# Kernel tuning notes

Measured on AMD Instinct MI355X. Metric: run time of the kernel, lower is better.

Reference implementation:

```python
import jax, jax.numpy as jnp
import numpy as np

CAPS_N, DIMS_N, ROUNDS = 10, 16, 3
IN_CAPS_N, IN_DIMS_N = 1152, 8
BATCH = 256
EPS = 1e-7  # keras backend.epsilon()


def squash(x, axis=-1):
    sq = jnp.sum(x * x, axis=axis, keepdims=True)
    return (sq / (1.0 + sq)) * x / jnp.sqrt(sq + EPS)


def setup_inputs() -> dict:
    key = jax.random.key(0)
    k1, k2 = jax.random.split(key)
    inputs = jax.random.normal(k1, (BATCH, IN_CAPS_N, IN_DIMS_N), dtype=jnp.float32)
    # glorot-ish scale for the transform weights
    W = jax.random.normal(k2, (CAPS_N, IN_CAPS_N, DIMS_N, IN_DIMS_N), dtype=jnp.float32) * 0.05
    return {"inputs": inputs, "W": W}


def reference(inputs, W):
    # u_hat[b,j,i,d] = W[j,i] @ inputs[b,i]  (per-pair prediction vectors)
    u_hat = jnp.einsum('jide,bie->bjid', W, inputs)  # [B, caps_n, in_caps_n, dims_n]
    B = inputs.shape[0]
    cc = jnp.zeros((B, CAPS_N, IN_CAPS_N), dtype=u_hat.dtype)  # routing logits
    v = None
    for r in range(ROUNDS):
        c = jax.nn.softmax(cc, axis=1)                    # softmax over output capsules
        s = jnp.einsum('bji,bjid->bjd', c, u_hat)         # weighted sum over input caps
        v = squash(s, axis=-1)                            # [B, caps_n, dims_n]
        if r != ROUNDS - 1:
            cc = cc + jnp.einsum('bjid,bjd->bji', u_hat, v)  # agreement
    return v
```

## Files before the change

kernel.cpp:

```cpp
#include <hip/hip_runtime.h>

#define B_N 256
#define IC_N 1152
#define J_N 10
#define D_N 16

typedef __attribute__((ext_vector_type(8))) short short8;
typedef __attribute__((ext_vector_type(4))) float floatx4;

union u4s8 { uint4 u; short8 s; };

__device__ __forceinline__ float bf_lo(unsigned int u){
  union { unsigned int i; float f; } c; c.i = u << 16; return c.f;
}
__device__ __forceinline__ float bf_hi(unsigned int u){
  union { unsigned int i; float f; } c; c.i = u & 0xffff0000u; return c.f;
}
__device__ __forceinline__ unsigned int rne16(float f){
  union { float ff; unsigned int i; } c; c.ff = f;
  return (c.i + 0x7FFFu + ((c.i >> 16) & 1u)) >> 16;
}
__device__ __forceinline__ unsigned int pack_rne(float lo, float hi){
  return rne16(lo) | (rne16(hi) << 16);
}
__device__ __forceinline__ unsigned int pack_trunc(float lo, float hi){
  union { float f; unsigned int u; } a, b; a.f = lo; b.f = hi;
  return __builtin_amdgcn_perm(b.u, a.u, 0x07060302u);
}

__global__ __launch_bounds__(256) void caps_prep(
    const float* __restrict__ W, const float* __restrict__ x,
    uint4* __restrict__ wsf, uint4* __restrict__ wcc2,
    uint4* __restrict__ xbf, float* __restrict__ vsum)
{
  __shared__ unsigned int tx[4][64 * 17];
  const int blk = blockIdx.x, tid = threadIdx.x;
  if (blk < 720) {
    const int t = blk * 256 + tid;
    if (t < B_N * J_N * D_N) vsum[t] = 0.f;
    const int d  = t & 15;
    const int ji = t >> 4;
    const int i  = ji % IC_N;
    const int j  = ji / IC_N;
    const float4* src = (const float4*)(W + ((size_t)t << 3));
    const float4 a = src[0], b = src[1];
    uint4 q;
    q.x = pack_rne(a.x, a.y); q.y = pack_rne(a.z, a.w);
    q.z = pack_rne(b.x, b.y); q.w = pack_rne(b.z, b.w);
    wsf[(j * 288 + (i >> 2)) * 64 + (i & 3) * 16 + d] = q;
  } else if (blk < 1440) {
    const int t2    = (blk - 720) * 256 + tid;
    const int lane  = t2 & 31;
    const int rest  = t2 >> 5;
    const int itile = rest % 72;
    const int je    = rest / 72;
    const int e     = je & 7;
    const int j     = je >> 3;
    const int i     = itile * 16 + (lane & 15);
    const int dbase = (lane >> 4) * 8;
    const float* src = W + (((size_t)(j * IC_N + i) * D_N + dbase) << 3) + e;
    uint4 q;
    q.x = pack_rne(src[0],  src[8]);  q.y = pack_rne(src[16], src[24]);
    q.z = pack_rne(src[32], src[40]); q.w = pack_rne(src[48], src[56]);
    wcc2[t2] = q;
  } else {
    const int xb = blk - 1440;
    const int b0 = (xb / 18) * 16;
    const int i0 = (xb % 18) * 64;
    #pragma unroll
    for (int r = 0; r < 4; ++r) {
      const int bl = r * 4 + (tid >> 6);
      const int il = tid & 63;
      const float4* sp = (const float4*)(x + ((size_t)((b0 + bl) * IC_N + i0 + il) << 3));
      const float4 a = sp[0], c = sp[1];
      tx[0][il * 17 + bl] = pack_rne(a.x, a.y);
      tx[1][il * 17 + bl] = pack_rne(a.z, a.w);
      tx[2][il * 17 + bl] = pack_rne(c.x, c.y);
      tx[3][il * 17 + bl] = pack_rne(c.z, c.w);
    }
    __syncthreads();
    #pragma unroll
    for (int it = 0; it < 4; ++it) {
      const int p  = it * 256 + tid;
      const int il = p >> 4, bl = p & 15;
      uint4 q;
      q.x = tx[0][il * 17 + bl]; q.y = tx[1][il * 17 + bl];
      q.z = tx[2][il * 17 + bl]; q.w = tx[3][il * 17 + bl];
      xbf[(size_t)(i0 + il) * 256 + b0 + bl] = q;
    }
  }
}

__global__ __launch_bounds__(640, 5) void caps_pass(
    const uint4* __restrict__ xbf,
    const uint4* __restrict__ wsf,
    const uint4* __restrict__ wcc2,
    const uint4* __restrict__ vsbf,
    float* __restrict__ s_part,
    const int round)
{
  __shared__ float ccl[10 * 32 * 17];

  const int tid  = threadIdx.x;
  const int wave = tid >> 6;
  const int lane = tid & 63;
  const int quad = lane >> 4;
  const int col  = lane & 15;
  const int b0   = blockIdx.x << 4;
  const int i0   = blockIdx.y << 5;

  if (round > 0) {
    short8 av = {0,0,0,0,0,0,0,0};
    if (quad < 2)
      av = *(const short8*)&vsbf[((size_t)(b0 + col) * J_N + wave) * 2 + quad];

    #pragma unroll
    for (int t2 = 0; t2 < 2; ++t2) {
      uint4 bvq[8];
      #pragma unroll
      for (int e = 0; e < 8; ++e) {
        uint4 q = {0u, 0u, 0u, 0u};
        if (lane < 32)
          q = wcc2[(((size_t)wave * 8 + e) * 72 + (blockIdx.y << 1) + t2) * 32 + lane];
        bvq[e] = q;
      }
      uint4 xr[4];
      #pragma unroll
      for (int r = 0; r < 4; ++r)
        xr[r] = xbf[(size_t)(i0 + t2 * 16 + col) * 256 + b0 + quad * 4 + r];

      floatx4 cc4 = {0.f, 0.f, 0.f, 0.f};
      #pragma unroll
      for (int e = 0; e < 8; ++e) {
        u4s8 bv; bv.u = bvq[e];
        floatx4 tf = {0.f, 0.f, 0.f, 0.f};
        tf = __builtin_amdgcn_mfma_f32_16x16x32_bf16(av, bv.s, tf, 0, 0, 0);
        #pragma unroll
        for (int r = 0; r < 4; ++r) {
          const unsigned int u = ((const unsigned int*)&xr[r])[e >> 1];
          const float xe = (e & 1) ? bf_hi(u) : bf_lo(u);
          cc4[r] += tf[r] * xe;
        }
      }
      #pragma unroll
      for (int r = 0; r < 4; ++r)
        ccl[(wave * 32 + t2 * 16 + col) * 17 + quad * 4 + r] = cc4[r];
    }
    __syncthreads();
    if (tid < 512) {
      const int i = tid >> 4, b = tid & 15;
      float cc[10];
      #pragma unroll
      for (int j = 0; j < 10; ++j) cc[j] = ccl[(j * 32 + i) * 17 + b];
      float m = cc[0];
      #pragma unroll
      for (int j = 1; j < 10; ++j) m = fmaxf(m, cc[j]);
      float den = 0.f;
      #pragma unroll
      for (int j = 0; j < 10; ++j) { cc[j] = __expf(cc[j] - m); den += cc[j]; }
      const float rd = __builtin_amdgcn_rcpf(den);
      #pragma unroll
      for (int j = 0; j < 10; ++j) ccl[(j * 32 + i) * 17 + b] = cc[j] * rd;
    }
    __syncthreads();
  }

  floatx4 acc = {0.f, 0.f, 0.f, 0.f};
  #pragma unroll
  for (int g = 0; g < 2; ++g) {
    uint4 xq[4], wf[4];
    float cv[4];
    #pragma unroll
    for (int k = 0; k < 4; ++k) {
      const int kt = g * 4 + k;
      const int il = kt * 4 + quad;
      xq[k] = xbf[(size_t)(i0 + il) * 256 + b0 + col];
      wf[k] = wsf[((size_t)wave * 288 + (blockIdx.y << 3) + kt) * 64 + lane];
      cv[k] = (round > 0) ? ccl[(wave * 32 + il) * 17 + col] : 0.1f;
    }
    #pragma unroll
    for (int k = 0; k < 4; ++k) {
      short8 af;
      unsigned int* aq = (unsigned int*)&af;
      aq[0] = pack_trunc(bf_lo(xq[k].x) * cv[k], bf_hi(xq[k].x) * cv[k]);
      aq[1] = pack_trunc(bf_lo(xq[k].y) * cv[k], bf_hi(xq[k].y) * cv[k]);
      aq[2] = pack_trunc(bf_lo(xq[k].z) * cv[k], bf_hi(xq[k].z) * cv[k]);
      aq[3] = pack_trunc(bf_lo(xq[k].w) * cv[k], bf_hi(xq[k].w) * cv[k]);
      u4s8 bw; bw.u = wf[k];
      acc = __builtin_amdgcn_mfma_f32_16x16x32_bf16(af, bw.s, acc, 0, 0, 0);
    }
  }
  float* sp = s_part + ((((size_t)blockIdx.x * 10 + wave) * 16 + quad * 4) * 36
                        + blockIdx.y) * 16 + col;
  #pragma unroll
  for (int r = 0; r < 4; ++r) sp[r * 576] = acc[r];
}

__global__ __launch_bounds__(256) void caps_squash(
    const float* __restrict__ s_part, float* __restrict__ vsum,
    unsigned int* __restrict__ vsbf_u, float* __restrict__ out, const int round)
{
  const int tid  = threadIdx.x;
  const int w    = tid >> 6;
  const int lane = tid & 63;
  const int bj   = blockIdx.x * 4 + w;
  const int b    = bj / 10, j = bj - b * 10;
  const int btile = b >> 4, brem = b & 15;
  const float* base = s_part + (((size_t)btile * 10 + j) * 16 + brem) * 576;
  float acc = 0.f;
  #pragma unroll
  for (int q = 0; q < 9; ++q) acc += base[q * 64 + lane];
  acc += __shfl_xor(acc, 16, 64);
  acc += __shfl_xor(acc, 32, 64);
  const float s = acc;
  float sq = s * s;
  sq += __shfl_xor(sq, 1, 16);
  sq += __shfl_xor(sq, 2, 16);
  sq += __shfl_xor(sq, 4, 16);
  sq += __shfl_xor(sq, 8, 16);
  const float coef = (sq / (1.f + sq)) * rsqrtf(sq + 1e-7f);
  const float v = coef * s;
  if (round < 2) {
    const float vprev = (lane < 16) ? vsum[bj * 16 + lane] : 0.f;
    const float vt = vprev + v;
    const float vtn = __shfl_down(vt, 1, 64);
    if (lane < 16) {
      vsum[bj * 16 + lane] = vt;
      if (!(lane & 1))
        vsbf_u[bj * 8 + (lane >> 1)] = pack_rne(vt, vtn);
    }
  } else if (lane < 16) {
    out[bj * 16 + lane] = v;
  }
}

extern "C" void kernel_launch(void* const* d_in, const int* in_sizes, int n_in,
                              void* d_out, int out_size, void* d_ws, size_t ws_size,
                              hipStream_t stream)
{
  const float* x = (const float*)d_in[0];
  const float* W = (const float*)d_in[1];

  uint4* wsf   = (uint4*)d_ws;
  uint4* wcc2  = wsf + 184320;
  uint4* xbf   = wcc2 + 184320;
  float* s_prt = (float*)(xbf + 294912);
  float* vsum  = s_prt + 1474560;
  unsigned int* vsbf_u = (unsigned int*)(vsum + 40960);

  caps_prep<<<dim3(1728), dim3(256), 0, stream>>>(W, x, wsf, wcc2,
                                                  (uint4*)xbf, vsum);
  for (int r = 0; r < 3; ++r) {
    caps_pass<<<dim3(16, 36), dim3(640), 0, stream>>>(
        xbf, wsf, wcc2, (const uint4*)vsbf_u, s_prt, r);
    caps_squash<<<dim3(640), dim3(256), 0, stream>>>(
        s_prt, vsum, vsbf_u, (float*)d_out, r);
  }
}
```

Measured before the change: 131.0 us.

## Halve input-capsule tile per block, add batch-major x copy, fuse W prep via LDS

caps_pass now handles 16 input capsules per block instead of 32, doubling the grid to 16x72 blocks for more parallelism, and writes twice as many partial sums that caps_squash reduces over 18 chunks instead of 9. A second batch-major bf16 copy of x is produced so the agreement step reads coalesced rows. The W preprocessing is restructured so one block loads a 16-capsule W tile once into LDS and emits both the wsf and wcc2 layouts, cutting strided global reads. The cost is extra workspace, a larger partial-sum buffer and more reduction traffic in squash.

```diff
diff --git a/kernel.cpp b/kernel.cpp
--- a/kernel.cpp
+++ b/kernel.cpp
@@ -31,40 +31,49 @@
 __global__ __launch_bounds__(256) void caps_prep(
     const float* __restrict__ W, const float* __restrict__ x,
     uint4* __restrict__ wsf, uint4* __restrict__ wcc2,
-    uint4* __restrict__ xbf, float* __restrict__ vsum)
-{
-  __shared__ unsigned int tx[4][64 * 17];
-  const int blk = blockIdx.x, tid = threadIdx.x;
-  if (blk < 720) {
-    const int t = blk * 256 + tid;
-    if (t < B_N * J_N * D_N) vsum[t] = 0.f;
-    const int d  = t & 15;
-    const int ji = t >> 4;
-    const int i  = ji % IC_N;
-    const int j  = ji / IC_N;
-    const float4* src = (const float4*)(W + ((size_t)t << 3));
-    const float4 a = src[0], b = src[1];
-    uint4 q;
-    q.x = pack_rne(a.x, a.y); q.y = pack_rne(a.z, a.w);
-    q.z = pack_rne(b.x, b.y); q.w = pack_rne(b.z, b.w);
-    wsf[(j * 288 + (i >> 2)) * 64 + (i & 3) * 16 + d] = q;
-  } else if (blk < 1440) {
-    const int t2    = (blk - 720) * 256 + tid;
-    const int lane  = t2 & 31;
-    const int rest  = t2 >> 5;
-    const int itile = rest % 72;
-    const int je    = rest / 72;
-    const int e     = je & 7;
-    const int j     = je >> 3;
-    const int i     = itile * 16 + (lane & 15);
-    const int dbase = (lane >> 4) * 8;
-    const float* src = W + (((size_t)(j * IC_N + i) * D_N + dbase) << 3) + e;
-    uint4 q;
-    q.x = pack_rne(src[0],  src[8]);  q.y = pack_rne(src[16], src[24]);
-    q.z = pack_rne(src[32], src[40]); q.w = pack_rne(src[48], src[56]);
-    wcc2[t2] = q;
+    uint4* __restrict__ xbf_ib, uint4* __restrict__ xbf_bi,
+    float* __restrict__ vsum)
+{
+  const int tid = threadIdx.x;
+  if (blockIdx.x < 720) {
+    __shared__ unsigned int lw[1024];
+    const int j = blockIdx.x / 72, itile = blockIdx.x % 72;
+    const float4* Wt = (const float4*)(W + ((size_t)(j * IC_N + itile * 16) << 7));
+    #pragma unroll
+    for (int h = 0; h < 2; ++h) {
+      const float4 f = Wt[h * 256 + tid];
+      lw[(h * 256 + tid) * 2]     = pack_rne(f.x, f.y);
+      lw[(h * 256 + tid) * 2 + 1] = pack_rne(f.z, f.w);
+    }
+    __syncthreads();
+    {
+      const int ktl = tid >> 6, lane = tid & 63;
+      const int base = (ktl * 4 + (lane >> 4)) * 64 + (lane & 15) * 4;
+      uint4 q;
+      q.x = lw[base]; q.y = lw[base + 1]; q.z = lw[base + 2]; q.w = lw[base + 3];
+      wsf[((size_t)j * 288 + itile * 4 + ktl) * 64 + lane] = q;
+    }
+    {
+      const int e = tid >> 5, lane2 = tid & 31;
+      const int il = lane2 & 15, dbase = (lane2 >> 4) * 8;
+      unsigned short h[8];
+      #pragma unroll
+      for (int k = 0; k < 8; ++k) {
+        const unsigned int u = lw[il * 64 + (dbase + k) * 4 + (e >> 1)];
+        h[k] = (e & 1) ? (unsigned short)(u >> 16) : (unsigned short)(u & 0xffffu);
+      }
+      uint4 q;
+      q.x = h[0] | ((unsigned int)h[1] << 16);
+      q.y = h[2] | ((unsigned int)h[3] << 16);
+      q.z = h[4] | ((unsigned int)h[5] << 16);
+      q.w = h[6] | ((unsigned int)h[7] << 16);
+      wcc2[(((size_t)j * 8 + e) * 72 + itile) * 32 + lane2] = q;
+    }
   } else {
-    const int xb = blk - 1440;
+    __shared__ unsigned int tx[4][64 * 17];
+    const int xb = blockIdx.x - 720;
+    const int t0 = xb * 256 + tid;
+    if (t0 < B_N * J_N * D_N) vsum[t0] = 0.f;
     const int b0 = (xb / 18) * 16;
     const int i0 = (xb % 18) * 64;
     #pragma unroll
@@ -73,10 +82,12 @@
       const int il = tid & 63;
       const float4* sp = (const float4*)(x + ((size_t)((b0 + bl) * IC_N + i0 + il) << 3));
       const float4 a = sp[0], c = sp[1];
-      tx[0][il * 17 + bl] = pack_rne(a.x, a.y);
-      tx[1][il * 17 + bl] = pack_rne(a.z, a.w);
-      tx[2][il * 17 + bl] = pack_rne(c.x, c.y);
-      tx[3][il * 17 + bl] = pack_rne(c.z, c.w);
+      uint4 q;
+      q.x = pack_rne(a.x, a.y); q.y = pack_rne(a.z, a.w);
+      q.z = pack_rne(c.x, c.y); q.w = pack_rne(c.z, c.w);
+      xbf_bi[(size_t)(b0 + bl) * IC_N + i0 + il] = q;
+      tx[0][il * 17 + bl] = q.x; tx[1][il * 17 + bl] = q.y;
+      tx[2][il * 17 + bl] = q.z; tx[3][il * 17 + bl] = q.w;
     }
     __syncthreads();
     #pragma unroll
@@ -86,20 +97,21 @@
       uint4 q;
       q.x = tx[0][il * 17 + bl]; q.y = tx[1][il * 17 + bl];
       q.z = tx[2][il * 17 + bl]; q.w = tx[3][il * 17 + bl];
-      xbf[(size_t)(i0 + il) * 256 + b0 + bl] = q;
+      xbf_ib[(size_t)(i0 + il) * 256 + b0 + bl] = q;
     }
   }
 }
 
 __global__ __launch_bounds__(640, 5) void caps_pass(
-    const uint4* __restrict__ xbf,
+    const uint4* __restrict__ xbf_ib,
+    const uint4* __restrict__ xbf_bi,
     const uint4* __restrict__ wsf,
     const uint4* __restrict__ wcc2,
     const uint4* __restrict__ vsbf,
     float* __restrict__ s_part,
     const int round)
 {
-  __shared__ float ccl[10 * 32 * 17];
+  __shared__ float ccl[10 * 16 * 17];
 
   const int tid  = threadIdx.x;
   const int wave = tid >> 6;
@@ -107,51 +119,48 @@
   const int quad = lane >> 4;
   const int col  = lane & 15;
   const int b0   = blockIdx.x << 4;
-  const int i0   = blockIdx.y << 5;
+  const int i0   = blockIdx.y << 4;
 
   if (round > 0) {
     short8 av = {0,0,0,0,0,0,0,0};
     if (quad < 2)
       av = *(const short8*)&vsbf[((size_t)(b0 + col) * J_N + wave) * 2 + quad];
 
-    #pragma unroll
-    for (int t2 = 0; t2 < 2; ++t2) {
-      uint4 bvq[8];
-      #pragma unroll
-      for (int e = 0; e < 8; ++e) {
-        uint4 q = {0u, 0u, 0u, 0u};
-        if (lane < 32)
-          q = wcc2[(((size_t)wave * 8 + e) * 72 + (blockIdx.y << 1) + t2) * 32 + lane];
-        bvq[e] = q;
+    uint4 bvq[8];
+    #pragma unroll
+    for (int e = 0; e < 8; ++e) {
+      uint4 q = {0u, 0u, 0u, 0u};
+      if (lane < 32)
+        q = wcc2[(((size_t)wave * 8 + e) * 72 + blockIdx.y) * 32 + lane];
+      bvq[e] = q;
+    }
+    uint4 xr[4];
+    #pragma unroll
+    for (int r = 0; r < 4; ++r)
+      xr[r] = xbf_bi[(size_t)(b0 + quad * 4 + r) * IC_N + i0 + col];
+
+    floatx4 cc4 = {0.f, 0.f, 0.f, 0.f};
+    #pragma unroll
+    for (int e = 0; e < 8; ++e) {
+      u4s8 bv; bv.u = bvq[e];
+      floatx4 tf = {0.f, 0.f, 0.f, 0.f};
+      tf = __builtin_amdgcn_mfma_f32_16x16x32_bf16(av, bv.s, tf, 0, 0, 0);
+      #pragma unroll
+      for (int r = 0; r < 4; ++r) {
+        const unsigned int u = ((const unsigned int*)&xr[r])[e >> 1];
+        const float xe = (e & 1) ? bf_hi(u) : bf_lo(u);
+        cc4[r] += tf[r] * xe;
       }
-      uint4 xr[4];
-      #pragma unroll
-      for (int r = 0; r < 4; ++r)
-        xr[r] = xbf[(size_t)(i0 + t2 * 16 + col) * 256 + b0 + quad * 4 + r];
-
-      floatx4 cc4 = {0.f, 0.f, 0.f, 0.f};
-      #pragma unroll
-      for (int e = 0; e < 8; ++e) {
-        u4s8 bv; bv.u = bvq[e];
-        floatx4 tf = {0.f, 0.f, 0.f, 0.f};
-        tf = __builtin_amdgcn_mfma_f32_16x16x32_bf16(av, bv.s, tf, 0, 0, 0);
-        #pragma unroll
-        for (int r = 0; r < 4; ++r) {
-          const unsigned int u = ((const unsigned int*)&xr[r])[e >> 1];
-          const float xe = (e & 1) ? bf_hi(u) : bf_lo(u);
-          cc4[r] += tf[r] * xe;
-        }
-      }
-      #pragma unroll
-      for (int r = 0; r < 4; ++r)
-        ccl[(wave * 32 + t2 * 16 + col) * 17 + quad * 4 + r] = cc4[r];
-    }
-    __syncthreads();
-    if (tid < 512) {
+    }
+    #pragma unroll
+    for (int r = 0; r < 4; ++r)
+      ccl[(wave * 16 + col) * 17 + quad * 4 + r] = cc4[r];
+    __syncthreads();
+    if (tid < 256) {
       const int i = tid >> 4, b = tid & 15;
       float cc[10];
       #pragma unroll
-      for (int j = 0; j < 10; ++j) cc[j] = ccl[(j * 32 + i) * 17 + b];
+      for (int j = 0; j < 10; ++j) cc[j] = ccl[(j * 16 + i) * 17 + b];
       float m = cc[0];
       #pragma unroll
       for (int j = 1; j < 10; ++j) m = fmaxf(m, cc[j]);
@@ -160,40 +169,36 @@
       for (int j = 0; j < 10; ++j) { cc[j] = __expf(cc[j] - m); den += cc[j]; }
       const float rd = __builtin_amdgcn_rcpf(den);
       #pragma unroll
-      for (int j = 0; j < 10; ++j) ccl[(j * 32 + i) * 17 + b] = cc[j] * rd;
+      for (int j = 0; j < 10; ++j) ccl[(j * 16 + i) * 17 + b] = cc[j] * rd;
     }
     __syncthreads();
   }
 
   floatx4 acc = {0.f, 0.f, 0.f, 0.f};
-  #pragma unroll
-  for (int g = 0; g < 2; ++g) {
-    uint4 xq[4], wf[4];
-    float cv[4];
-    #pragma unroll
-    for (int k = 0; k < 4; ++k) {
-      const int kt = g * 4 + k;
-      const int il = kt * 4 + quad;
-      xq[k] = xbf[(size_t)(i0 + il) * 256 + b0 + col];
-      wf[k] = wsf[((size_t)wave * 288 + (blockIdx.y << 3) + kt) * 64 + lane];
-      cv[k] = (round > 0) ? ccl[(wave * 32 + il) * 17 + col] : 0.1f;
-    }
-    #pragma unroll
-    for (int k = 0; k < 4; ++k) {
-      short8 af;
-      unsigned int* aq = (unsigned int*)&af;
-      aq[0] = pack_trunc(bf_lo(xq[k].x) * cv[k], bf_hi(xq[k].x) * cv[k]);
-      aq[1] = pack_trunc(bf_lo(xq[k].y) * cv[k], bf_hi(xq[k].y) * cv[k]);
-      aq[2] = pack_trunc(bf_lo(xq[k].z) * cv[k], bf_hi(xq[k].z) * cv[k]);
-      aq[3] = pack_trunc(bf_lo(xq[k].w) * cv[k], bf_hi(xq[k].w) * cv[k]);
-      u4s8 bw; bw.u = wf[k];
-      acc = __builtin_amdgcn_mfma_f32_16x16x32_bf16(af, bw.s, acc, 0, 0, 0);
-    }
-  }
-  float* sp = s_part + ((((size_t)blockIdx.x * 10 + wave) * 16 + quad * 4) * 36
+  uint4 xq[4], wf[4];
+  float cv[4];
+  #pragma unroll
+  for (int kt = 0; kt < 4; ++kt) {
+    const int il = kt * 4 + quad;
+    xq[kt] = xbf_ib[(size_t)(i0 + il) * 256 + b0 + col];
+    wf[kt] = wsf[((size_t)wave * 288 + (blockIdx.y << 2) + kt) * 64 + lane];
+    cv[kt] = (round > 0) ? ccl[(wave * 16 + il) * 17 + col] : 0.1f;
+  }
+  #pragma unroll
+  for (int kt = 0; kt < 4; ++kt) {
+    short8 af;
+    unsigned int* aq = (unsigned int*)&af;
+    aq[0] = pack_trunc(bf_lo(xq[kt].x) * cv[kt], bf_hi(xq[kt].x) * cv[kt]);
+    aq[1] = pack_trunc(bf_lo(xq[kt].y) * cv[kt], bf_hi(xq[kt].y) * cv[kt]);
+    aq[2] = pack_trunc(bf_lo(xq[kt].z) * cv[kt], bf_hi(xq[kt].z) * cv[kt]);
+    aq[3] = pack_trunc(bf_lo(xq[kt].w) * cv[kt], bf_hi(xq[kt].w) * cv[kt]);
+    u4s8 bw; bw.u = wf[kt];
+    acc = __builtin_amdgcn_mfma_f32_16x16x32_bf16(af, bw.s, acc, 0, 0, 0);
+  }
+  float* sp = s_part + ((((size_t)blockIdx.x * 10 + wave) * 16 + quad * 4) * 72
                         + blockIdx.y) * 16 + col;
   #pragma unroll
-  for (int r = 0; r < 4; ++r) sp[r * 576] = acc[r];
+  for (int r = 0; r < 4; ++r) sp[(size_t)r * 72 * 16] = acc[r];
 }
 
 __global__ __launch_bounds__(256) void caps_squash(
@@ -206,10 +211,10 @@
   const int bj   = blockIdx.x * 4 + w;
   const int b    = bj / 10, j = bj - b * 10;
   const int btile = b >> 4, brem = b & 15;
-  const float* base = s_part + (((size_t)btile * 10 + j) * 16 + brem) * 576;
+  const float* base = s_part + (((size_t)btile * 10 + j) * 16 + brem) * 1152;
   float acc = 0.f;
   #pragma unroll
-  for (int q = 0; q < 9; ++q) acc += base[q * 64 + lane];
+  for (int q = 0; q < 18; ++q) acc += base[q * 64 + lane];
   acc += __shfl_xor(acc, 16, 64);
   acc += __shfl_xor(acc, 32, 64);
   const float s = acc;
@@ -241,18 +246,19 @@
   const float* x = (const float*)d_in[0];
   const float* W = (const float*)d_in[1];
 
-  uint4* wsf   = (uint4*)d_ws;
-  uint4* wcc2  = wsf + 184320;
-  uint4* xbf   = wcc2 + 184320;
-  float* s_prt = (float*)(xbf + 294912);
-  float* vsum  = s_prt + 1474560;
+  uint4* wsf    = (uint4*)d_ws;
+  uint4* wcc2   = wsf + 184320;
+  uint4* xbf_ib = wcc2 + 184320;
+  uint4* xbf_bi = xbf_ib + 294912;
+  float* s_prt  = (float*)(xbf_bi + 294912);
+  float* vsum   = s_prt + 2949120;
   unsigned int* vsbf_u = (unsigned int*)(vsum + 40960);
 
-  caps_prep<<<dim3(1728), dim3(256), 0, stream>>>(W, x, wsf, wcc2,
-                                                  (uint4*)xbf, vsum);
+  caps_prep<<<dim3(1008), dim3(256), 0, stream>>>(W, x, wsf, wcc2,
+                                                  xbf_ib, xbf_bi, vsum);
   for (int r = 0; r < 3; ++r) {
-    caps_pass<<<dim3(16, 36), dim3(640), 0, stream>>>(
-        xbf, wsf, wcc2, (const uint4*)vsbf_u, s_prt, r);
+    caps_pass<<<dim3(16, 72), dim3(640), 0, stream>>>(
+        xbf_ib, xbf_bi, wsf, wcc2, (const uint4*)vsbf_u, s_prt, r);
     caps_squash<<<dim3(640), dim3(256), 0, stream>>>(
         s_prt, vsum, vsbf_u, (float*)d_out, r);
   }
```

Result: faster. 115.8 us (-11.6%).
